# Performance work log

Hardware: AMD Instinct MI355X
Metric: run time of the kernel (lower is better)

The kernel has to match this reference:

```python
import jax, jax.numpy as jnp
import numpy as np

H = 16  # hidden_size
D = 32  # input_size == output_size
B = 2048
T = 512


def _leaky(x):
    return jnp.where(x >= 0, x, 0.01 * x)  # nn.LeakyReLU default slope


def _lstm_cell(x, h, c, Wih, Whh, bih, bhh):
    # torch.nn.LSTMCell gate order: i, f, g, o
    g = x @ Wih.T + h @ Whh.T + bih + bhh  # [B, 4H]
    i, f, gg, o = jnp.split(g, 4, axis=-1)
    i = jax.nn.sigmoid(i)
    f = jax.nn.sigmoid(f)
    gg = jnp.tanh(gg)
    o = jax.nn.sigmoid(o)
    c = f * c + i * gg
    h = o * jnp.tanh(c)
    return h, c


def setup_inputs() -> dict:
    key = jax.random.key(0)
    ks = jax.random.split(key, 20)
    s = 1.0 / np.sqrt(H)
    u = lambda k, shape: jax.random.uniform(k, shape, jnp.float32, -s, s)
    return {
        "seq": jax.random.normal(ks[0], (B, T, D), jnp.float32),
        "pre_w1": u(ks[1], (H, D)), "pre_b1": u(ks[2], (H,)),
        "pre_w2": u(ks[3], (H, H)), "pre_b2": u(ks[4], (H,)),
        "pre_w3": u(ks[5], (H, H)), "pre_b3": u(ks[6], (H,)),
        "enc_Wih": u(ks[7], (4 * H, H)), "enc_Whh": u(ks[8], (4 * H, H)),
        "enc_bih": u(ks[9], (4 * H,)), "enc_bhh": u(ks[10], (4 * H,)),
        "h2l_w1": u(ks[11], (H, H)), "h2l_b1": u(ks[12], (H,)),
        "h2l_w2": u(ks[13], (H, H)), "h2l_b2": u(ks[14], (H,)),
        "post_w": u(ks[15], (D, H)), "post_b": u(ks[16], (D,)),
    }


def reference(seq, pre_w1, pre_b1, pre_w2, pre_b2, pre_w3, pre_b3,
              enc_Wih, enc_Whh, enc_bih, enc_bhh,
              h2l_w1, h2l_b1, h2l_w2, h2l_b2, post_w, post_b):
    Bx = seq.shape[0]
    # pre MLP: Linear -> LeakyReLU -> Linear -> LeakyReLU -> Linear
    x = _leaky(seq @ pre_w1.T + pre_b1)
    x = _leaky(x @ pre_w2.T + pre_b2)
    x = x @ pre_w3.T + pre_b3  # [B, T, H]

    start0 = x[:, -1, :]
    h0 = jnp.zeros((Bx, H), seq.dtype)
    c0 = jnp.zeros((Bx, H), seq.dtype)

    # encoder loop over time (serial)
    def enc_step(carry, xt):
        h, c = carry
        h, c = _lstm_cell(xt, h, c, enc_Wih, enc_Whh, enc_bih, enc_bhh)
        return (h, c), None

    (h, c), _ = jax.lax.scan(enc_step, (h0, c0), jnp.swapaxes(x, 0, 1))

    # decoder loop (note: source reuses self.encoder cell here)
    def dec_step(carry, _):
        h, c, start = carry
        h, c = _lstm_cell(start, h, c, enc_Wih, enc_Whh, enc_bih, enc_bhh)
        start = _leaky(h @ h2l_w1.T + h2l_b1) @ h2l_w2.T + h2l_b2
        out = h @ post_w.T + post_b  # [B, D]
        return (h, c, start), out

    _, outs = jax.lax.scan(dec_step, (h, c, start0), None, length=seq.shape[1])
    # outputs[:, -1 - i] = out_i  ->  reverse time, then [B, T, D]
    outputs = jnp.swapaxes(outs[::-1], 0, 1)
    return (outputs, outputs)
```

## Files before the change

### kernel.cpp

```cpp
#include <hip/hip_runtime.h>

#define T_LEN 512
#define OSTRIDE ((size_t)2048 * 512 * 32)

__device__ __forceinline__ float rlf(float v, int l) {
  return __int_as_float(__builtin_amdgcn_readlane(__float_as_int(v), l));
}
#define QB(v, pat) __int_as_float(__builtin_amdgcn_mov_dpp(__float_as_int(v), (pat), 0xF, 0xF, false))

__global__ __launch_bounds__(256) void prenet_kernel(
    const float* __restrict__ seq,
    const float* __restrict__ w1, const float* __restrict__ b1,
    const float* __restrict__ w2, const float* __restrict__ b2,
    const float* __restrict__ w3, const float* __restrict__ b3,
    float* __restrict__ xws) {
  const int tid = threadIdx.x;
  const size_t r = (size_t)blockIdx.x * 256 + tid;
  const float* sp = seq + r * 32;

  float in[32];
#pragma unroll
  for (int q = 0; q < 8; ++q) {
    float4 v = ((const float4*)sp)[q];
    in[q * 4 + 0] = v.x;
    in[q * 4 + 1] = v.y;
    in[q * 4 + 2] = v.z;
    in[q * 4 + 3] = v.w;
  }

  float y1[16];
#pragma unroll
  for (int j = 0; j < 16; ++j) {
    float a0 = b1[j], a1 = 0.f, a2 = 0.f, a3 = 0.f;
#pragma unroll
    for (int k = 0; k < 32; k += 4) {
      a0 = __builtin_fmaf(w1[j * 32 + k + 0], in[k + 0], a0);
      a1 = __builtin_fmaf(w1[j * 32 + k + 1], in[k + 1], a1);
      a2 = __builtin_fmaf(w1[j * 32 + k + 2], in[k + 2], a2);
      a3 = __builtin_fmaf(w1[j * 32 + k + 3], in[k + 3], a3);
    }
    float s = (a0 + a1) + (a2 + a3);
    y1[j] = s >= 0.f ? s : 0.01f * s;
  }

  float y2[16];
#pragma unroll
  for (int j = 0; j < 16; ++j) {
    float a0 = b2[j], a1 = 0.f, a2 = 0.f, a3 = 0.f;
#pragma unroll
    for (int k = 0; k < 16; k += 4) {
      a0 = __builtin_fmaf(w2[j * 16 + k + 0], y1[k + 0], a0);
      a1 = __builtin_fmaf(w2[j * 16 + k + 1], y1[k + 1], a1);
      a2 = __builtin_fmaf(w2[j * 16 + k + 2], y1[k + 2], a2);
      a3 = __builtin_fmaf(w2[j * 16 + k + 3], y1[k + 3], a3);
    }
    float s = (a0 + a1) + (a2 + a3);
    y2[j] = s >= 0.f ? s : 0.01f * s;
  }

  float y3[16];
#pragma unroll
  for (int j = 0; j < 16; ++j) {
    float a0 = b3[j], a1 = 0.f, a2 = 0.f, a3 = 0.f;
#pragma unroll
    for (int k = 0; k < 16; k += 4) {
      a0 = __builtin_fmaf(w3[j * 16 + k + 0], y2[k + 0], a0);
      a1 = __builtin_fmaf(w3[j * 16 + k + 1], y2[k + 1], a1);
      a2 = __builtin_fmaf(w3[j * 16 + k + 2], y2[k + 2], a2);
      a3 = __builtin_fmaf(w3[j * 16 + k + 3], y2[k + 3], a3);
    }
    y3[j] = (a0 + a1) + (a2 + a3);
  }

  float* op = xws + r * 16;
#pragma unroll
  for (int q = 0; q < 4; ++q)
    ((float4*)op)[q] =
        make_float4(y3[q * 4 + 0], y3[q * 4 + 1], y3[q * 4 + 2], y3[q * 4 + 3]);
}

#define CELL(WX, XA, BB)                                                    \
  do {                                                                      \
    float a0 = (BB), a1 = 0.f, a2 = 0.f, a3 = 0.f;                          \
    _Pragma("unroll") for (int k = 0; k < 16; k += 4) {                     \
      a0 = __builtin_fmaf(WX[k + 0], XA[k + 0], a0);                        \
      a1 = __builtin_fmaf(WX[k + 1], XA[k + 1], a1);                        \
      a2 = __builtin_fmaf(WX[k + 2], XA[k + 2], a2);                        \
      a3 = __builtin_fmaf(WX[k + 3], XA[k + 3], a3);                        \
    }                                                                       \
    _Pragma("unroll") for (int k = 0; k < 16; k += 4) {                     \
      a0 = __builtin_fmaf(whhr[k + 0], hk[k + 0], a0);                      \
      a1 = __builtin_fmaf(whhr[k + 1], hk[k + 1], a1);                      \
      a2 = __builtin_fmaf(whhr[k + 2], hk[k + 2], a2);                      \
      a3 = __builtin_fmaf(whhr[k + 3], hk[k + 3], a3);                      \
    }                                                                       \
    float g = (a0 + a1) + (a2 + a3);                                        \
    float ee = __expf(g);                                                   \
    float rr = __builtin_amdgcn_rcpf(1.0f + ee);                            \
    float act = __builtin_fmaf(sa, rr, sb);                                 \
    float ii = QB(act, 0x00);                                               \
    float ff = QB(act, 0x55);                                               \
    float gg = QB(act, 0xAA);                                               \
    float oo = QB(act, 0xFF);                                               \
    c = __builtin_fmaf(ff, c, ii * gg);                                     \
    float th = __builtin_fmaf(                                              \
        -2.0f, __builtin_amdgcn_rcpf(1.0f + __expf(c + c)), 1.0f);          \
    h = oo * th;                                                            \
    _Pragma("unroll") for (int k = 0; k < 16; ++k) hk[k] = rlf(h, 4 * k);   \
  } while (0)

__global__ __launch_bounds__(256) void lstm_rec_kernel(
    const float* __restrict__ Wih, const float* __restrict__ Whh,
    const float* __restrict__ bih, const float* __restrict__ bhh,
    const float* __restrict__ hw1, const float* __restrict__ hb1,
    const float* __restrict__ hw2, const float* __restrict__ hb2,
    const float* __restrict__ pw, const float* __restrict__ pb,
    const float* __restrict__ xws, float* __restrict__ out) {
  const int lane = threadIdx.x & 63;
  const int bu =
      __builtin_amdgcn_readfirstlane(blockIdx.x * 4 + (threadIdx.x >> 6));
  const int hr = lane >> 2;
  const int gi = (lane & 3) * 16 + hr;
  const bool isT = (lane & 3) == 2;

  const float sK = isT ? 2.0f : -1.0f;
  const float sa = isT ? -2.0f : 1.0f;
  const float sb = isT ? 1.0f : 0.0f;

  float wihr[16], whhr[16];
#pragma unroll
  for (int k = 0; k < 16; ++k) {
    wihr[k] = Wih[gi * 16 + k] * sK;
    whhr[k] = Whh[gi * 16 + k] * sK;
  }
  const float bias = (bih[gi] + bhh[gi]) * sK;

  float h = 0.f, c = 0.f;
  float hk[16];
#pragma unroll
  for (int k = 0; k < 16; ++k) hk[k] = 0.f;

  const float* xb = xws + (size_t)bu * (T_LEN * 16);

  float xA[16], xB[16];
#pragma unroll
  for (int k = 0; k < 16; ++k) xA[k] = xb[k];
  for (int t = 0; t < T_LEN; t += 2) {
    const float* n1 = xb + (size_t)(t + 1) * 16;
#pragma unroll
    for (int k = 0; k < 16; ++k) xB[k] = n1[k];
    CELL(wihr, xA, bias);
    const int t2 = (t + 2 < T_LEN) ? (t + 2) : (T_LEN - 1);
    const float* n2 = xb + (size_t)t2 * 16;
#pragma unroll
    for (int k = 0; k < 16; ++k) xA[k] = n2[k];
    CELL(wihr, xB, bias);
  }

  const int mrow = (lane < 32) ? lane : (lane & 15);
  const float* msrc = (lane < 32) ? (pw + mrow * 16) : (hw1 + mrow * 16);
  const float mbias = (lane < 32) ? pb[mrow] : hb1[mrow];
  const float sl = (lane < 32) ? 1.0f : 0.01f;
  float mr[16];
#pragma unroll
  for (int k = 0; k < 16; ++k) mr[k] = msrc[k];

  float Mr[16];
#pragma unroll
  for (int k = 0; k < 16; ++k) Mr[k] = 0.f;
#pragma unroll
  for (int j = 0; j < 16; ++j) {
#pragma unroll
    for (int k = 0; k < 16; ++k)
      Mr[k] = __builtin_fmaf(wihr[j], hw2[j * 16 + k], Mr[k]);
  }
  float mbias2 = bias;
#pragma unroll
  for (int j = 0; j < 16; ++j)
    mbias2 = __builtin_fmaf(wihr[j], hb2[j], mbias2);

  float xk[16];
  {
    const float* src = xb + (size_t)(T_LEN - 1) * 16;
#pragma unroll
    for (int k = 0; k < 16; ++k) xk[k] = src[k];
  }

  float uk[16];
  const size_t obase = (size_t)bu * (T_LEN * 32) + (lane & 31);

  CELL(wihr, xk, bias);

  for (int t = 0; t < T_LEN; ++t) {
    float p0 = mbias, p1 = 0.f, p2 = 0.f, p3 = 0.f;
#pragma unroll
    for (int k = 0; k < 16; k += 4) {
      p0 = __builtin_fmaf(mr[k + 0], hk[k + 0], p0);
      p1 = __builtin_fmaf(mr[k + 1], hk[k + 1], p1);
      p2 = __builtin_fmaf(mr[k + 2], hk[k + 2], p2);
      p3 = __builtin_fmaf(mr[k + 3], hk[k + 3], p3);
    }
    float y0 = (p0 + p1) + (p2 + p3);
    float yv = fmaxf(y0, y0 * sl);

    if (lane < 32) {
      const size_t off = obase + (size_t)(T_LEN - 1 - t) * 32;
      out[off] = yv;
      out[off + OSTRIDE] = yv;
    }

    if (t + 1 < T_LEN) {
#pragma unroll
      for (int k = 0; k < 16; ++k) uk[k] = rlf(yv, 32 + k);
      CELL(Mr, uk, mbias2);
    }
  }
}

extern "C" void kernel_launch(void* const* d_in, const int* in_sizes, int n_in,
                              void* d_out, int out_size, void* d_ws, size_t ws_size,
                              hipStream_t stream) {
  const float* seq = (const float*)d_in[0];
  const float* pre_w1 = (const float*)d_in[1];
  const float* pre_b1 = (const float*)d_in[2];
  const float* pre_w2 = (const float*)d_in[3];
  const float* pre_b2 = (const float*)d_in[4];
  const float* pre_w3 = (const float*)d_in[5];
  const float* pre_b3 = (const float*)d_in[6];
  const float* enc_Wih = (const float*)d_in[7];
  const float* enc_Whh = (const float*)d_in[8];
  const float* enc_bih = (const float*)d_in[9];
  const float* enc_bhh = (const float*)d_in[10];
  const float* h2l_w1 = (const float*)d_in[11];
  const float* h2l_b1 = (const float*)d_in[12];
  const float* h2l_w2 = (const float*)d_in[13];
  const float* h2l_b2 = (const float*)d_in[14];
  const float* post_w = (const float*)d_in[15];
  const float* post_b = (const float*)d_in[16];

  float* xws = (float*)d_ws;

  prenet_kernel<<<dim3(4096), dim3(256), 0, stream>>>(
      seq, pre_w1, pre_b1, pre_w2, pre_b2, pre_w3, pre_b3, xws);

  lstm_rec_kernel<<<dim3(512), dim3(256), 0, stream>>>(
      enc_Wih, enc_Whh, enc_bih, enc_bhh, h2l_w1, h2l_b1, h2l_w2, h2l_b2,
      post_w, post_b, xws, (float*)d_out);
}
```

Measured before the change: 783.0 us.

## Precompute encoder input projections in prenet and prefetch them in recurrence

```diff
diff --git a/kernel.cpp b/kernel.cpp
--- a/kernel.cpp
+++ b/kernel.cpp
@@ -8,16 +8,12 @@
 }
 #define QB(v, pat) __int_as_float(__builtin_amdgcn_mov_dpp(__float_as_int(v), (pat), 0xF, 0xF, false))
 
-__global__ __launch_bounds__(256) void prenet_kernel(
-    const float* __restrict__ seq,
+__device__ __forceinline__ void prenet_row(
+    const float* __restrict__ sp,
     const float* __restrict__ w1, const float* __restrict__ b1,
     const float* __restrict__ w2, const float* __restrict__ b2,
     const float* __restrict__ w3, const float* __restrict__ b3,
-    float* __restrict__ xws) {
-  const int tid = threadIdx.x;
-  const size_t r = (size_t)blockIdx.x * 256 + tid;
-  const float* sp = seq + r * 32;
-
+    float y3[16]) {
   float in[32];
 #pragma unroll
   for (int q = 0; q < 8; ++q) {
@@ -58,7 +54,6 @@
     y2[j] = s >= 0.f ? s : 0.01f * s;
   }
 
-  float y3[16];
 #pragma unroll
   for (int j = 0; j < 16; ++j) {
     float a0 = b3[j], a1 = 0.f, a2 = 0.f, a3 = 0.f;
@@ -71,13 +66,79 @@
     }
     y3[j] = (a0 + a1) + (a2 + a3);
   }
-
-  float* op = xws + r * 16;
-#pragma unroll
-  for (int q = 0; q < 4; ++q)
-    ((float4*)op)[q] =
-        make_float4(y3[q * 4 + 0], y3[q * 4 + 1], y3[q * 4 + 2], y3[q * 4 + 3]);
-}
+}
+
+__global__ __launch_bounds__(256) void prenet_z_kernel(
+    const float* __restrict__ seq,
+    const float* __restrict__ w1, const float* __restrict__ b1,
+    const float* __restrict__ w2, const float* __restrict__ b2,
+    const float* __restrict__ w3, const float* __restrict__ b3,
+    const float* __restrict__ Wih, const float* __restrict__ bih,
+    const float* __restrict__ bhh,
+    float* __restrict__ z, float* __restrict__ xstart) {
+  const size_t r = (size_t)blockIdx.x * 256 + threadIdx.x;
+  float y3[16];
+  prenet_row(seq + r * 32, w1, b1, w2, b2, w3, b3, y3);
+
+  float* zp = z + r * 64;
+#pragma unroll
+  for (int j = 0; j < 64; j += 4) {
+    float4 o;
+    float* op = (float*)&o;
+#pragma unroll
+    for (int jj = 0; jj < 4; ++jj) {
+      const int g = j + jj;
+      const float sK = ((g >> 4) == 2) ? 2.0f : -1.0f;
+      float a0 = bih[g] + bhh[g], a1 = 0.f, a2 = 0.f, a3 = 0.f;
+#pragma unroll
+      for (int k = 0; k < 16; k += 4) {
+        a0 = __builtin_fmaf(Wih[g * 16 + k + 0], y3[k + 0], a0);
+        a1 = __builtin_fmaf(Wih[g * 16 + k + 1], y3[k + 1], a1);
+        a2 = __builtin_fmaf(Wih[g * 16 + k + 2], y3[k + 2], a2);
+        a3 = __builtin_fmaf(Wih[g * 16 + k + 3], y3[k + 3], a3);
+      }
+      op[jj] = sK * ((a0 + a1) + (a2 + a3));
+    }
+    ((float4*)zp)[j >> 2] = o;
+  }
+
+  if ((r & (T_LEN - 1)) == (T_LEN - 1)) {
+    float* xs = xstart + (r >> 9) * 16;
+#pragma unroll
+    for (int q = 0; q < 4; ++q)
+      ((float4*)xs)[q] = make_float4(y3[q * 4 + 0], y3[q * 4 + 1],
+                                     y3[q * 4 + 2], y3[q * 4 + 3]);
+  }
+}
+
+#define ACTBODY()                                                           \
+  do {                                                                      \
+    float ee = __expf(g);                                                   \
+    float rr = __builtin_amdgcn_rcpf(1.0f + ee);                            \
+    float act = __builtin_fmaf(sa, rr, sb);                                 \
+    float ii = QB(act, 0x00);                                               \
+    float ff = QB(act, 0x55);                                               \
+    float gg = QB(act, 0xAA);                                               \
+    float oo = QB(act, 0xFF);                                               \
+    c = __builtin_fmaf(ff, c, ii * gg);                                     \
+    float th = __builtin_fmaf(                                              \
+        -2.0f, __builtin_amdgcn_rcpf(1.0f + __expf(c + c)), 1.0f);          \
+    h = oo * th;                                                            \
+    _Pragma("unroll") for (int k = 0; k < 16; ++k) hk[k] = rlf(h, 4 * k);   \
+  } while (0)
+
+#define CELLZ(ZV)                                                           \
+  do {                                                                      \
+    float a0 = (ZV), a1 = 0.f, a2 = 0.f, a3 = 0.f;                          \
+    _Pragma("unroll") for (int k = 0; k < 16; k += 4) {                     \
+      a0 = __builtin_fmaf(whhr[k + 0], hk[k + 0], a0);                      \
+      a1 = __builtin_fmaf(whhr[k + 1], hk[k + 1], a1);                      \
+      a2 = __builtin_fmaf(whhr[k + 2], hk[k + 2], a2);                      \
+      a3 = __builtin_fmaf(whhr[k + 3], hk[k + 3], a3);                      \
+    }                                                                       \
+    float g = (a0 + a1) + (a2 + a3);                                        \
+    ACTBODY();                                                              \
+  } while (0)
 
 #define CELL(WX, XA, BB)                                                    \
   do {                                                                      \
@@ -95,19 +156,131 @@
       a3 = __builtin_fmaf(whhr[k + 3], hk[k + 3], a3);                      \
     }                                                                       \
     float g = (a0 + a1) + (a2 + a3);                                        \
-    float ee = __expf(g);                                                   \
-    float rr = __builtin_amdgcn_rcpf(1.0f + ee);                            \
-    float act = __builtin_fmaf(sa, rr, sb);                                 \
-    float ii = QB(act, 0x00);                                               \
-    float ff = QB(act, 0x55);                                               \
-    float gg = QB(act, 0xAA);                                               \
-    float oo = QB(act, 0xFF);                                               \
-    c = __builtin_fmaf(ff, c, ii * gg);                                     \
-    float th = __builtin_fmaf(                                              \
-        -2.0f, __builtin_amdgcn_rcpf(1.0f + __expf(c + c)), 1.0f);          \
-    h = oo * th;                                                            \
-    _Pragma("unroll") for (int k = 0; k < 16; ++k) hk[k] = rlf(h, 4 * k);   \
+    ACTBODY();                                                              \
   } while (0)
+
+__global__ __launch_bounds__(256) void lstm_rec_z_kernel(
+    const float* __restrict__ Whh, const float* __restrict__ Wih,
+    const float* __restrict__ bih, const float* __restrict__ bhh,
+    const float* __restrict__ hw1, const float* __restrict__ hb1,
+    const float* __restrict__ hw2, const float* __restrict__ hb2,
+    const float* __restrict__ pw, const float* __restrict__ pb,
+    const float* __restrict__ z, const float* __restrict__ xstart,
+    float* __restrict__ out) {
+  const int lane = threadIdx.x & 63;
+  const int bu =
+      __builtin_amdgcn_readfirstlane(blockIdx.x * 4 + (threadIdx.x >> 6));
+  const int hr = lane >> 2;
+  const int gi = (lane & 3) * 16 + hr;
+  const bool isT = (lane & 3) == 2;
+
+  const float sK = isT ? 2.0f : -1.0f;
+  const float sa = isT ? -2.0f : 1.0f;
+  const float sb = isT ? 1.0f : 0.0f;
+
+  float whhr[16];
+#pragma unroll
+  for (int k = 0; k < 16; ++k) whhr[k] = Whh[gi * 16 + k] * sK;
+
+  float h = 0.f, c = 0.f;
+  float hk[16];
+#pragma unroll
+  for (int k = 0; k < 16; ++k) hk[k] = 0.f;
+
+  const float* zb = z + (size_t)bu * (T_LEN * 64) + gi;
+  float zq[8];
+#pragma unroll
+  for (int u = 0; u < 8; ++u) zq[u] = zb[(size_t)u * 64];
+
+  for (int t0 = 0; t0 < T_LEN; t0 += 8) {
+#pragma unroll
+    for (int u = 0; u < 8; ++u) {
+      CELLZ(zq[u]);
+      int tn = t0 + u + 8;
+      tn = tn < T_LEN ? tn : (T_LEN - 1);
+      zq[u] = zb[(size_t)tn * 64];
+    }
+  }
+
+  float wihr[16];
+#pragma unroll
+  for (int k = 0; k < 16; ++k) wihr[k] = Wih[gi * 16 + k] * sK;
+  const float bias = (bih[gi] + bhh[gi]) * sK;
+
+  const int mrow = (lane < 32) ? lane : (lane & 15);
+  const float* msrc = (lane < 32) ? (pw + mrow * 16) : (hw1 + mrow * 16);
+  const float mbias = (lane < 32) ? pb[mrow] : hb1[mrow];
+  const float sl = (lane < 32) ? 1.0f : 0.01f;
+  float mr[16];
+#pragma unroll
+  for (int k = 0; k < 16; ++k) mr[k] = msrc[k];
+
+  float Mr[16];
+#pragma unroll
+  for (int k = 0; k < 16; ++k) Mr[k] = 0.f;
+#pragma unroll
+  for (int j = 0; j < 16; ++j) {
+#pragma unroll
+    for (int k = 0; k < 16; ++k)
+      Mr[k] = __builtin_fmaf(wihr[j], hw2[j * 16 + k], Mr[k]);
+  }
+  float mbias2 = bias;
+#pragma unroll
+  for (int j = 0; j < 16; ++j) mbias2 = __builtin_fmaf(wihr[j], hb2[j], mbias2);
+
+  float xk[16];
+  {
+    const float* src = xstart + (size_t)bu * 16;
+#pragma unroll
+    for (int k = 0; k < 16; ++k) xk[k] = src[k];
+  }
+
+  float uk[16];
+  const size_t obase = (size_t)bu * (T_LEN * 32) + (lane & 31);
+
+  CELL(wihr, xk, bias);
+
+  for (int t = 0; t < T_LEN; ++t) {
+    float p0 = mbias, p1 = 0.f, p2 = 0.f, p3 = 0.f;
+#pragma unroll
+    for (int k = 0; k < 16; k += 4) {
+      p0 = __builtin_fmaf(mr[k + 0], hk[k + 0], p0);
+      p1 = __builtin_fmaf(mr[k + 1], hk[k + 1], p1);
+      p2 = __builtin_fmaf(mr[k + 2], hk[k + 2], p2);
+      p3 = __builtin_fmaf(mr[k + 3], hk[k + 3], p3);
+    }
+    float y0 = (p0 + p1) + (p2 + p3);
+    float yv = fmaxf(y0, y0 * sl);
+
+    if (lane < 32) {
+      const size_t off = obase + (size_t)(T_LEN - 1 - t) * 32;
+      out[off] = yv;
+      out[off + OSTRIDE] = yv;
+    }
+
+    if (t + 1 < T_LEN) {
+#pragma unroll
+      for (int k = 0; k < 16; ++k) uk[k] = rlf(yv, 32 + k);
+      CELL(Mr, uk, mbias2);
+    }
+  }
+}
+
+__global__ __launch_bounds__(256) void prenet_kernel(
+    const float* __restrict__ seq,
+    const float* __restrict__ w1, const float* __restrict__ b1,
+    const float* __restrict__ w2, const float* __restrict__ b2,
+    const float* __restrict__ w3, const float* __restrict__ b3,
+    float* __restrict__ xws) {
+  const size_t r = (size_t)blockIdx.x * 256 + threadIdx.x;
+  float y3[16];
+  prenet_row(seq + r * 32, w1, b1, w2, b2, w3, b3, y3);
+  float* op = xws + r * 16;
+#pragma unroll
+  for (int q = 0; q < 4; ++q)
+    ((float4*)op)[q] =
+        make_float4(y3[q * 4 + 0], y3[q * 4 + 1], y3[q * 4 + 2], y3[q * 4 + 3]);
+}
 
 __global__ __launch_bounds__(256) void lstm_rec_kernel(
     const float* __restrict__ Wih, const float* __restrict__ Whh,
@@ -176,8 +349,7 @@
   }
   float mbias2 = bias;
 #pragma unroll
-  for (int j = 0; j < 16; ++j)
-    mbias2 = __builtin_fmaf(wihr[j], hb2[j], mbias2);
+  for (int j = 0; j < 16; ++j) mbias2 = __builtin_fmaf(wihr[j], hb2[j], mbias2);
 
   float xk[16];
   {
@@ -238,12 +410,28 @@
   const float* post_w = (const float*)d_in[15];
   const float* post_b = (const float*)d_in[16];
 
-  float* xws = (float*)d_ws;
-
-  prenet_kernel<<<dim3(4096), dim3(256), 0, stream>>>(
-      seq, pre_w1, pre_b1, pre_w2, pre_b2, pre_w3, pre_b3, xws);
-
-  lstm_rec_kernel<<<dim3(512), dim3(256), 0, stream>>>(
-      enc_Wih, enc_Whh, enc_bih, enc_bhh, h2l_w1, h2l_b1, h2l_w2, h2l_b2,
-      post_w, post_b, xws, (float*)d_out);
-}
+  const size_t zbytes = (size_t)1048576 * 64 * 4;
+  const size_t need = zbytes + (size_t)2048 * 16 * 4;
+
+  if (ws_size >= need) {
+    float* z = (float*)d_ws;
+    float* xstart = (float*)((char*)d_ws + zbytes);
+
+    prenet_z_kernel<<<dim3(4096), dim3(256), 0, stream>>>(
+        seq, pre_w1, pre_b1, pre_w2, pre_b2, pre_w3, pre_b3, enc_Wih, enc_bih,
+        enc_bhh, z, xstart);
+
+    lstm_rec_z_kernel<<<dim3(512), dim3(256), 0, stream>>>(
+        enc_Whh, enc_Wih, enc_bih, enc_bhh, h2l_w1, h2l_b1, h2l_w2, h2l_b2,
+        post_w, post_b, z, xstart, (float*)d_out);
+  } else {
+    float* xws = (float*)d_ws;
+
+    prenet_kernel<<<dim3(4096), dim3(256), 0, stream>>>(
+        seq, pre_w1, pre_b1, pre_w2, pre_b2, pre_w3, pre_b3, xws);
+
+    lstm_rec_kernel<<<dim3(512), dim3(256), 0, stream>>>(
+        enc_Wih, enc_Whh, enc_bih, enc_bhh, h2l_w1, h2l_b1, h2l_w2, h2l_b2,
+        post_w, post_b, xws, (float*)d_out);
+  }
+}
```

Result: slower. 898.9 us (+14.8%).
